# Kernel tuning notes

Hardware: AMD Instinct MI355X
Metric: run time of the kernel (lower is better)

Reference implementation:

```python
import jax, jax.numpy as jnp
import numpy as np
from jax import lax

K = 3       # kernel_conv
STRIDE = 1
PAD = 1


def setup_inputs() -> dict:
    key = jax.random.key(0)
    ks = jax.random.split(key, 11)
    b, n, H, W = 8, 64, 128, 128
    m = 64
    kk = K * K
    return {
        "x": jax.random.normal(ks[0], (b, n, H, W), jnp.float32),
        "atw1": jax.random.uniform(ks[1], (b, kk, H, W), jnp.float32),  # sigmoid-range attention1 output
        "weight": jax.random.normal(ks[2], (m, n, K, K), jnp.float32) * 0.05,
        "a2_w1": jax.random.normal(ks[3], (kk, n), jnp.float32) * 0.1,
        "a2_b1": jax.random.normal(ks[4], (kk,), jnp.float32) * 0.1,
        "a2_w2": jax.random.normal(ks[5], (kk, kk), jnp.float32) * 0.1,
        "a2_b2": jax.random.normal(ks[6], (kk,), jnp.float32) * 0.1,
        "a3_w1": jax.random.normal(ks[7], (m, n), jnp.float32) * 0.1,
        "a3_b1": jax.random.normal(ks[8], (m,), jnp.float32) * 0.1,
        "a3_w2": jax.random.normal(ks[9], (m, m), jnp.float32) * 0.1,
        "a3_b2": jax.random.normal(ks[10], (m,), jnp.float32) * 0.1,
    }


def reference(x, atw1, weight, a2_w1, a2_b1, a2_w2, a2_b2, a3_w1, a3_b1, a3_w2, a3_b2):
    b, n, H, W = x.shape
    m = weight.shape[0]
    kk = K * K
    n_H = 1 + (H + 2 * PAD - K) // STRIDE
    n_W = 1 + (W + 2 * PAD - K) // STRIDE
    P = n_H * n_W

    # F.unfold(x, k, stride, padding): [b, n*k*k, P] with channel-major ordering (c, kh, kw)
    patches = lax.conv_general_dilated_patches(
        x, (K, K), (STRIDE, STRIDE), [(PAD, PAD), (PAD, PAD)])  # [b, n*kk, n_H, n_W]
    kx = patches.reshape(b, n, kk, P)

    # attention2: global avg pool + two 1x1 convs -> per-batch per-tap ratio [b, kk]
    g = x.mean(axis=(2, 3))                                   # [b, n]
    ratio = jax.nn.relu(g @ a2_w1.T + a2_b1) @ a2_w2.T + a2_b2  # [b, kk]

    # per-pixel per-tap weight (broadcast over input channels, as the torch repeat/view does)
    a = atw1.reshape(b, kk, P) * ratio[:, :, None]            # [b, kk, P]
    wx = kx * a[:, None, :, :]                                # [b, n, kk, P]

    # dynamic-weighted im2col matmul with static conv weight
    w = weight.reshape(m, n, kk)
    y = jnp.einsum('bctp,mct->bmp', wx, w)                    # [b, m, P]

    # attention3 bias: global avg pool + two 1x1 convs -> [b, m]
    bias = jax.nn.relu(g @ a3_w1.T + a3_b1) @ a3_w2.T + a3_b2
    y = y + bias[:, :, None]

    # F.fold with kernel 1 is a reshape back to the spatial grid
    return y.reshape(b, m, n_H, n_W)
```

## Files before the change

### kernel.cpp

```cpp
#include <hip/hip_runtime.h>

typedef __attribute__((ext_vector_type(8))) short short8;
typedef __attribute__((ext_vector_type(4))) float f32x4;

#define HH 128
#define WW 128
#define TW 16
#define TH 4
#define HALOW 18
#define HALOH 6
#define NPIX (HALOW * HALOH)
#define NGROUP (TH / 2)

__device__ inline unsigned short f2bf(float f) {
    unsigned int u = __builtin_bit_cast(unsigned int, f);
    u += 0x7fffu + ((u >> 16) & 1u);
    return (unsigned short)(u >> 16);
}

__global__ __launch_bounds__(256) void prep_kernel(
    const float* __restrict__ x, const float* __restrict__ wgt,
    unsigned short* __restrict__ xT, float* __restrict__ partials,
    unsigned short* __restrict__ W3) {
    const int id = blockIdx.x;
    const int tid = threadIdx.x;
    {
        int i = id * 256 + tid;
        if (i < 64 * 64 * 9) {
            int j = i & 7, rest = i >> 3;
            int m = rest & 63; rest >>= 6;
            int lk = rest & 3; rest >>= 2;
            int ks = rest & 1, t = rest >> 1;
            int c = ks * 32 + lk * 8 + j;
            W3[i] = f2bf(wgt[(m * 64 + c) * 9 + t]);
        }
    }
    const int b = id & 7, pt = id >> 3;
    const int p0 = pt * 64;
    __shared__ unsigned int lt[64 * 33];
    __shared__ float red[8][32][2];

    const int px = tid & 63, cp0 = tid >> 6;
    const float* xb = x + (size_t)b * 64 * (HH * WW) + p0 + px;
    #pragma unroll
    for (int i = 0; i < 8; ++i) {
        int cp = cp0 + 4 * i;
        float v0 = xb[(size_t)(2 * cp) * (HH * WW)];
        float v1 = xb[(size_t)(2 * cp + 1) * (HH * WW)];
        lt[px * 33 + cp] = (unsigned)f2bf(v0) | ((unsigned)f2bf(v1) << 16);
    }
    __syncthreads();
    #pragma unroll
    for (int it = 0; it < 2; ++it) {
        int idx = it * 256 + tid;
        int p = idx >> 3, ch = idx & 7;
        int o = p * 33 + ch * 4;
        uint4 v = make_uint4(lt[o], lt[o + 1], lt[o + 2], lt[o + 3]);
        *(uint4*)(xT + ((size_t)(b * (HH * WW) + p0 + p) * 64 + ch * 8)) = v;
    }
    {
        int cp = tid & 31, grp = tid >> 5;
        float s0 = 0.f, s1 = 0.f;
        #pragma unroll
        for (int j2 = 0; j2 < 8; ++j2) {
            unsigned u = lt[(grp * 8 + j2) * 33 + cp];
            s0 += __builtin_bit_cast(float, u << 16);
            s1 += __builtin_bit_cast(float, u & 0xffff0000u);
        }
        red[grp][cp][0] = s0;
        red[grp][cp][1] = s1;
    }
    __syncthreads();
    if (tid < 64) {
        float s = 0.f;
        #pragma unroll
        for (int g2 = 0; g2 < 8; ++g2) s += red[g2][tid >> 1][tid & 1];
        partials[(size_t)(b * 256 + pt) * 64 + tid] = s;
    }
}

__global__ __launch_bounds__(256) void mlp_kernel(
    const float* __restrict__ partials,
    const float* __restrict__ a2w1, const float* __restrict__ a2b1,
    const float* __restrict__ a2w2, const float* __restrict__ a2b2,
    const float* __restrict__ a3w1, const float* __restrict__ a3b1,
    const float* __restrict__ a3w2, const float* __restrict__ a3b2,
    float* __restrict__ ratio, float* __restrict__ bias) {
    int b = blockIdx.x;
    int tid = threadIdx.x;
    int t = tid & 63, is = tid >> 6;
    float s = 0.f;
    #pragma unroll 8
    for (int k = 0; k < 64; ++k)
        s += partials[(size_t)(b * 256 + is + 4 * k) * 64 + t];
    __shared__ float rb[4][64];
    __shared__ float gs[64], h2[9], h3[64];
    rb[is][t] = s;
    __syncthreads();
    if (tid < 64)
        gs[t] = (rb[0][t] + rb[1][t] + rb[2][t] + rb[3][t]) * (1.f / (HH * WW));
    __syncthreads();
    if (tid < 64) {
        float s3 = 0.f;
        #pragma unroll 8
        for (int i = 0; i < 64; ++i) s3 += gs[i] * a3w1[t * 64 + i];
        h3[t] = fmaxf(s3 + a3b1[t], 0.f);
        if (t < 9) {
            float s2 = 0.f;
            #pragma unroll 8
            for (int i = 0; i < 64; ++i) s2 += gs[i] * a2w1[t * 64 + i];
            h2[t] = fmaxf(s2 + a2b1[t], 0.f);
        }
    }
    __syncthreads();
    if (tid < 64) {
        float o = 0.f;
        #pragma unroll 8
        for (int i = 0; i < 64; ++i) o += h3[i] * a3w2[t * 64 + i];
        bias[b * 64 + t] = o + a3b2[t];
        if (t < 9) {
            float r = 0.f;
            #pragma unroll
            for (int i = 0; i < 9; ++i) r += h2[i] * a2w2[t * 9 + i];
            ratio[b * 9 + t] = r + a2b2[t];
        }
    }
}

__global__ __launch_bounds__(256, 4) void main_kernel(
    const unsigned short* __restrict__ xT, const float* __restrict__ atw1,
    const unsigned short* __restrict__ W3, const float* __restrict__ ratio,
    const float* __restrict__ bias, float* __restrict__ out) {
    const int id = blockIdx.x;
    const int b = id & 7;
    const int rem = id >> 3;
    const int tY = rem >> 3;
    const int tX = rem & 7;
    const int tid = threadIdx.x;
    const int lane = tid & 63;
    const int wtile = tid >> 6;
    const int lm = lane & 15;
    const int lk = lane >> 4;
    const int px0 = tX * TW, py0 = tY * TH;

    __shared__ char xsc[NPIX * 128];
    __shared__ float alds[9][TH][TW];

    #pragma unroll
    for (int it = 0; it < 4; ++it) {
        int idx = it * 256 + tid;
        if (idx < NPIX * 8) {
            int pix = idx >> 3, ch = idx & 7;
            int yy = pix / HALOW;
            int xx = pix - yy * HALOW;
            int gy = py0 + yy - 1, gx = px0 + xx - 1;
            uint4 v = make_uint4(0u, 0u, 0u, 0u);
            if (gy >= 0 && gy < HH && gx >= 0 && gx < WW)
                v = *(const uint4*)(xT + ((size_t)((b * HH + gy) * WW + gx) * 64 + ch * 8));
            *(uint4*)(xsc + pix * 128 + ((ch * 16) ^ ((pix & 7) << 4))) = v;
        }
    }

    #pragma unroll
    for (int i = tid; i < 9 * TH * TW; i += 256) {
        int t = i / (TH * TW);
        int rem2 = i - t * (TH * TW);
        int rr = rem2 >> 4, cc = rem2 & 15;
        alds[0][0][i] = atw1[((size_t)(b * 9 + t) * HH + py0 + rr) * WW + px0 + cc]
                        * ratio[b * 9 + t];
    }

    short8 wfrag[9][2];
    {
        const short8* W3v = (const short8*)W3;
        #pragma unroll
        for (int t = 0; t < 9; ++t)
            #pragma unroll
            for (int ks = 0; ks < 2; ++ks)
                wfrag[t][ks] = W3v[(((t * 2 + ks) * 4 + lk) * 64) + wtile * 16 + lm];
    }

    float biasr[4];
    #pragma unroll
    for (int q = 0; q < 4; ++q) biasr[q] = bias[b * 64 + wtile * 16 + lk * 4 + q];

    __syncthreads();

    #pragma unroll 1
    for (int g2 = 0; g2 < NGROUP; ++g2) {
        const int r0 = g2 * 2;
        float av[2][9];
        #pragma unroll
        for (int rr = 0; rr < 2; ++rr)
            #pragma unroll
            for (int t = 0; t < 9; ++t) av[rr][t] = alds[t][r0 + rr][lm];

        f32x4 yac[2];
        #pragma unroll
        for (int rr = 0; rr < 2; ++rr) yac[rr] = (f32x4){0.f, 0.f, 0.f, 0.f};

        #pragma unroll
        for (int hl = 0; hl < 4; ++hl) {
            const int pixr = (r0 + hl) * HALOW + lm;
            short8 bf[3][2];
            #pragma unroll
            for (int dx = 0; dx < 3; ++dx) {
                const int pix = pixr + dx;
                const int sw = (pix & 7) << 4;
                const char* bp2 = xsc + pix * 128;
                #pragma unroll
                for (int ks = 0; ks < 2; ++ks)
                    bf[dx][ks] = __builtin_bit_cast(short8,
                        *(const uint4*)(bp2 + ((ks * 64 + lk * 16) ^ sw)));
            }
            #pragma unroll
            for (int dy = 0; dy < 3; ++dy) {
                const int r = hl - dy;
                if (r < 0 || r > 1) continue;
                #pragma unroll
                for (int dx = 0; dx < 3; ++dx) {
                    const int t = dy * 3 + dx;
                    f32x4 z = {0.f, 0.f, 0.f, 0.f};
                    z = __builtin_amdgcn_mfma_f32_16x16x32_bf16(wfrag[t][0], bf[dx][0], z, 0, 0, 0);
                    z = __builtin_amdgcn_mfma_f32_16x16x32_bf16(wfrag[t][1], bf[dx][1], z, 0, 0, 0);
                    #pragma unroll
                    for (int q = 0; q < 4; ++q) yac[r][q] = fmaf(av[r][t], z[q], yac[r][q]);
                }
            }
        }
        #pragma unroll
        for (int rr = 0; rr < 2; ++rr) {
            const int pyg = py0 + r0 + rr;
            #pragma unroll
            for (int q = 0; q < 4; ++q) {
                int m = wtile * 16 + lk * 4 + q;
                out[((size_t)(b * 64 + m) * HH + pyg) * WW + px0 + lm] = yac[rr][q] + biasr[q];
            }
        }
    }
}

extern "C" void kernel_launch(void* const* d_in, const int* in_sizes, int n_in,
                              void* d_out, int out_size, void* d_ws, size_t ws_size,
                              hipStream_t stream) {
    const float* x    = (const float*)d_in[0];
    const float* atw1 = (const float*)d_in[1];
    const float* wgt  = (const float*)d_in[2];
    const float* a2w1 = (const float*)d_in[3];
    const float* a2b1 = (const float*)d_in[4];
    const float* a2w2 = (const float*)d_in[5];
    const float* a2b2 = (const float*)d_in[6];
    const float* a3w1 = (const float*)d_in[7];
    const float* a3b1 = (const float*)d_in[8];
    const float* a3w2 = (const float*)d_in[9];
    const float* a3b2 = (const float*)d_in[10];
    float* out = (float*)d_out;

    float* ws = (float*)d_ws;
    float* ratio = ws;
    float* bias  = ws + 128;
    unsigned short* W3 = (unsigned short*)(ws + 1024);
    float* partials = ws + 19456;
    unsigned short* xT = (unsigned short*)(ws + 150528);

    prep_kernel<<<dim3(2048), dim3(256), 0, stream>>>(x, wgt, xT, partials, W3);
    mlp_kernel<<<dim3(8), dim3(256), 0, stream>>>(partials, a2w1, a2b1, a2w2, a2b2,
                                                  a3w1, a3b1, a3w2, a3b2, ratio, bias);
    main_kernel<<<dim3(2048), dim3(256), 0, stream>>>(xT, atw1, W3, ratio, bias, out);
}
```

Baseline: 44.04 us.

## Replace LDS halo tiling with direct global loads over persistent row-strip tasks

Removes the shared-memory halo tile and the atw1 staging buffer. Each block now loops over four 1x16-pixel row tasks and loads the 3x3 neighbourhood of bf16 channels straight from global memory, relying on L1/L2 to supply the halo reuse. The weight fragments are loaded once per block and reused across four tasks, and the occupancy hint drops from 4 to 3 blocks per SM. The trade is more global or cache traffic and longer load latency for each MFMA, since the halo data is re-read three times per row instead of once from LDS.

```diff
diff --git a/kernel.cpp b/kernel.cpp
--- a/kernel.cpp
+++ b/kernel.cpp
@@ -5,12 +5,6 @@
 
 #define HH 128
 #define WW 128
-#define TW 16
-#define TH 4
-#define HALOW 18
-#define HALOH 6
-#define NPIX (HALOW * HALOH)
-#define NGROUP (TH / 2)
 
 __device__ inline unsigned short f2bf(float f) {
     unsigned int u = __builtin_bit_cast(unsigned int, f);
@@ -127,48 +121,18 @@
     }
 }
 
-__global__ __launch_bounds__(256, 4) void main_kernel(
+__global__ __launch_bounds__(256, 3) void main_kernel(
     const unsigned short* __restrict__ xT, const float* __restrict__ atw1,
     const unsigned short* __restrict__ W3, const float* __restrict__ ratio,
     const float* __restrict__ bias, float* __restrict__ out) {
     const int id = blockIdx.x;
     const int b = id & 7;
-    const int rem = id >> 3;
-    const int tY = rem >> 3;
-    const int tX = rem & 7;
+    const int j = id >> 3;
     const int tid = threadIdx.x;
     const int lane = tid & 63;
     const int wtile = tid >> 6;
     const int lm = lane & 15;
     const int lk = lane >> 4;
-    const int px0 = tX * TW, py0 = tY * TH;
-
-    __shared__ char xsc[NPIX * 128];
-    __shared__ float alds[9][TH][TW];
-
-    #pragma unroll
-    for (int it = 0; it < 4; ++it) {
-        int idx = it * 256 + tid;
-        if (idx < NPIX * 8) {
-            int pix = idx >> 3, ch = idx & 7;
-            int yy = pix / HALOW;
-            int xx = pix - yy * HALOW;
-            int gy = py0 + yy - 1, gx = px0 + xx - 1;
-            uint4 v = make_uint4(0u, 0u, 0u, 0u);
-            if (gy >= 0 && gy < HH && gx >= 0 && gx < WW)
-                v = *(const uint4*)(xT + ((size_t)((b * HH + gy) * WW + gx) * 64 + ch * 8));
-            *(uint4*)(xsc + pix * 128 + ((ch * 16) ^ ((pix & 7) << 4))) = v;
-        }
-    }
-
-    #pragma unroll
-    for (int i = tid; i < 9 * TH * TW; i += 256) {
-        int t = i / (TH * TW);
-        int rem2 = i - t * (TH * TW);
-        int rr = rem2 >> 4, cc = rem2 & 15;
-        alds[0][0][i] = atw1[((size_t)(b * 9 + t) * HH + py0 + rr) * WW + px0 + cc]
-                        * ratio[b * 9 + t];
-    }
 
     short8 wfrag[9][2];
     {
@@ -179,64 +143,64 @@
             for (int ks = 0; ks < 2; ++ks)
                 wfrag[t][ks] = W3v[(((t * 2 + ks) * 4 + lk) * 64) + wtile * 16 + lm];
     }
-
+    float rat[9];
+    #pragma unroll
+    for (int t = 0; t < 9; ++t) rat[t] = ratio[b * 9 + t];
     float biasr[4];
     #pragma unroll
     for (int q = 0; q < 4; ++q) biasr[q] = bias[b * 64 + wtile * 16 + lk * 4 + q];
 
-    __syncthreads();
+    const unsigned short* xb = xT + (size_t)b * (HH * WW) * 64;
+    const float* ab = atw1 + (size_t)b * 9 * (HH * WW);
+    float* ob = out + (size_t)b * 64 * (HH * WW);
 
     #pragma unroll 1
-    for (int g2 = 0; g2 < NGROUP; ++g2) {
-        const int r0 = g2 * 2;
-        float av[2][9];
-        #pragma unroll
-        for (int rr = 0; rr < 2; ++rr)
-            #pragma unroll
-            for (int t = 0; t < 9; ++t) av[rr][t] = alds[t][r0 + rr][lm];
-
-        f32x4 yac[2];
-        #pragma unroll
-        for (int rr = 0; rr < 2; ++rr) yac[rr] = (f32x4){0.f, 0.f, 0.f, 0.f};
-
-        #pragma unroll
-        for (int hl = 0; hl < 4; ++hl) {
-            const int pixr = (r0 + hl) * HALOW + lm;
+    for (int it = 0; it < 4; ++it) {
+        const int task = j + it * 256;
+        const int y = task >> 3;
+        const int x0 = (task & 7) * 16;
+        const int gx = x0 + lm;
+
+        float av[9];
+        #pragma unroll
+        for (int t = 0; t < 9; ++t)
+            av[t] = ab[(size_t)t * (HH * WW) + y * WW + gx] * rat[t];
+
+        f32x4 yac = {0.f, 0.f, 0.f, 0.f};
+
+        #pragma unroll
+        for (int dy = 0; dy < 3; ++dy) {
+            const int gy = y + dy - 1;
+            const bool rowok = (gy >= 0) && (gy < HH);
             short8 bf[3][2];
             #pragma unroll
             for (int dx = 0; dx < 3; ++dx) {
-                const int pix = pixr + dx;
-                const int sw = (pix & 7) << 4;
-                const char* bp2 = xsc + pix * 128;
+                const int gxx = gx + dx - 1;
+                const bool ok = rowok && (gxx >= 0) && (gxx < WW);
+                const uint4* p = (const uint4*)(xb + (size_t)(gy * WW + gxx) * 64);
                 #pragma unroll
-                for (int ks = 0; ks < 2; ++ks)
-                    bf[dx][ks] = __builtin_bit_cast(short8,
-                        *(const uint4*)(bp2 + ((ks * 64 + lk * 16) ^ sw)));
-            }
-            #pragma unroll
-            for (int dy = 0; dy < 3; ++dy) {
-                const int r = hl - dy;
-                if (r < 0 || r > 1) continue;
-                #pragma unroll
-                for (int dx = 0; dx < 3; ++dx) {
-                    const int t = dy * 3 + dx;
-                    f32x4 z = {0.f, 0.f, 0.f, 0.f};
-                    z = __builtin_amdgcn_mfma_f32_16x16x32_bf16(wfrag[t][0], bf[dx][0], z, 0, 0, 0);
-                    z = __builtin_amdgcn_mfma_f32_16x16x32_bf16(wfrag[t][1], bf[dx][1], z, 0, 0, 0);
-                    #pragma unroll
-                    for (int q = 0; q < 4; ++q) yac[r][q] = fmaf(av[r][t], z[q], yac[r][q]);
+                for (int ks = 0; ks < 2; ++ks) {
+                    uint4 v = make_uint4(0u, 0u, 0u, 0u);
+                    if (ok) v = p[ks * 4 + lk];
+                    bf[dx][ks] = __builtin_bit_cast(short8, v);
                 }
             }
-        }
-        #pragma unroll
-        for (int rr = 0; rr < 2; ++rr) {
-            const int pyg = py0 + r0 + rr;
-            #pragma unroll
-            for (int q = 0; q < 4; ++q) {
-                int m = wtile * 16 + lk * 4 + q;
-                out[((size_t)(b * 64 + m) * HH + pyg) * WW + px0 + lm] = yac[rr][q] + biasr[q];
+            #pragma unroll
+            for (int dx = 0; dx < 3; ++dx) {
+                const int t = dy * 3 + dx;
+                f32x4 z = {0.f, 0.f, 0.f, 0.f};
+                z = __builtin_amdgcn_mfma_f32_16x16x32_bf16(wfrag[t][0], bf[dx][0], z, 0, 0, 0);
+                z = __builtin_amdgcn_mfma_f32_16x16x32_bf16(wfrag[t][1], bf[dx][1], z, 0, 0, 0);
+                #pragma unroll
+                for (int q = 0; q < 4; ++q) yac[q] = fmaf(av[t], z[q], yac[q]);
             }
         }
+        #pragma unroll
+        for (int q = 0; q < 4; ++q) {
+            int m = wtile * 16 + lk * 4 + q;
+            ob[((size_t)m * HH + y) * WW + gx] = yac[q] + biasr[q];
+        }
+        __builtin_amdgcn_s_barrier();
     }
 }
 
```

Result: slower. 99.33 us (+125.6%).

## Make main kernel persistent over four tiles with register-staged double buffering

Applied to the files above, without the earlier changes.

Each block of the main kernel now processes four consecutive spatial tiles instead of one, and the grid shrinks to 512 blocks. The next tile's input halo and attention weights are prefetched into registers while MFMAs run on the current tile, then written to a second LDS buffer. This is meant to hide global load latency and amortise the per-block weight-fragment and bias loads. In exchange, LDS use doubles, the launch bound drops to 2 blocks per CU, and the small grid may underfill the CUs.

```diff
diff --git a/kernel.cpp b/kernel.cpp
--- a/kernel.cpp
+++ b/kernel.cpp
@@ -10,7 +10,8 @@
 #define HALOW 18
 #define HALOH 6
 #define NPIX (HALOW * HALOH)
-#define NGROUP (TH / 2)
+#define XSB (NPIX * 128)
+#define NA (9 * TH * TW)
 
 __device__ inline unsigned short f2bf(float f) {
     unsigned int u = __builtin_bit_cast(unsigned int, f);
@@ -127,48 +128,21 @@
     }
 }
 
-__global__ __launch_bounds__(256, 4) void main_kernel(
+__global__ __launch_bounds__(256, 2) void main_kernel(
     const unsigned short* __restrict__ xT, const float* __restrict__ atw1,
     const unsigned short* __restrict__ W3, const float* __restrict__ ratio,
     const float* __restrict__ bias, float* __restrict__ out) {
     const int id = blockIdx.x;
     const int b = id & 7;
-    const int rem = id >> 3;
-    const int tY = rem >> 3;
-    const int tX = rem & 7;
+    const int j = id >> 3;
     const int tid = threadIdx.x;
     const int lane = tid & 63;
     const int wtile = tid >> 6;
     const int lm = lane & 15;
     const int lk = lane >> 4;
-    const int px0 = tX * TW, py0 = tY * TH;
-
-    __shared__ char xsc[NPIX * 128];
-    __shared__ float alds[9][TH][TW];
-
-    #pragma unroll
-    for (int it = 0; it < 4; ++it) {
-        int idx = it * 256 + tid;
-        if (idx < NPIX * 8) {
-            int pix = idx >> 3, ch = idx & 7;
-            int yy = pix / HALOW;
-            int xx = pix - yy * HALOW;
-            int gy = py0 + yy - 1, gx = px0 + xx - 1;
-            uint4 v = make_uint4(0u, 0u, 0u, 0u);
-            if (gy >= 0 && gy < HH && gx >= 0 && gx < WW)
-                v = *(const uint4*)(xT + ((size_t)((b * HH + gy) * WW + gx) * 64 + ch * 8));
-            *(uint4*)(xsc + pix * 128 + ((ch * 16) ^ ((pix & 7) << 4))) = v;
-        }
-    }
-
-    #pragma unroll
-    for (int i = tid; i < 9 * TH * TW; i += 256) {
-        int t = i / (TH * TW);
-        int rem2 = i - t * (TH * TW);
-        int rr = rem2 >> 4, cc = rem2 & 15;
-        alds[0][0][i] = atw1[((size_t)(b * 9 + t) * HH + py0 + rr) * WW + px0 + cc]
-                        * ratio[b * 9 + t];
-    }
+
+    __shared__ char xsc[2][XSB];
+    __shared__ float alds[2][NA];
 
     short8 wfrag[9][2];
     {
@@ -179,64 +153,130 @@
             for (int ks = 0; ks < 2; ++ks)
                 wfrag[t][ks] = W3v[(((t * 2 + ks) * 4 + lk) * 64) + wtile * 16 + lm];
     }
-
     float biasr[4];
     #pragma unroll
     for (int q = 0; q < 4; ++q) biasr[q] = bias[b * 64 + wtile * 16 + lk * 4 + q];
 
+    const unsigned short* xb = xT + (size_t)b * (HH * WW) * 64;
+    const float* ab = atw1 + (size_t)b * 9 * (HH * WW);
+    const float* rg = ratio + b * 9;
+    float* ob = out + (size_t)b * 64 * (HH * WW);
+
+    uint4 sx[4];
+    float sa[3];
+
+    auto LOADT = [&](int task) {
+        const int py0 = (task >> 3) * TH, px0 = (task & 7) * TW;
+        #pragma unroll
+        for (int i = 0; i < 4; ++i) {
+            int idx = i * 256 + tid;
+            uint4 v = make_uint4(0u, 0u, 0u, 0u);
+            if (idx < NPIX * 8) {
+                int pix = idx >> 3, ch = idx & 7;
+                int yy = pix / HALOW;
+                int xx = pix - yy * HALOW;
+                int gy = py0 + yy - 1, gx = px0 + xx - 1;
+                if (gy >= 0 && gy < HH && gx >= 0 && gx < WW)
+                    v = *(const uint4*)(xb + ((size_t)(gy * WW + gx) * 64 + ch * 8));
+            }
+            sx[i] = v;
+        }
+        #pragma unroll
+        for (int i = 0; i < 3; ++i) {
+            int idx = i * 256 + tid;
+            float v = 0.f;
+            if (idx < NA) {
+                int t = idx >> 6, rem = idx & 63;
+                int rr = rem >> 4, cc = rem & 15;
+                v = ab[(size_t)t * (HH * WW) + (py0 + rr) * WW + px0 + cc] * rg[t];
+            }
+            sa[i] = v;
+        }
+    };
+    auto DSWRITE = [&](int bi) {
+        #pragma unroll
+        for (int i = 0; i < 4; ++i) {
+            int idx = i * 256 + tid;
+            if (idx < NPIX * 8) {
+                int pix = idx >> 3, ch = idx & 7;
+                *(uint4*)(&xsc[bi][pix * 128 + ((ch * 16) ^ ((pix & 7) << 4))]) = sx[i];
+            }
+        }
+        #pragma unroll
+        for (int i = 0; i < 3; ++i) {
+            int idx = i * 256 + tid;
+            if (idx < NA) alds[bi][idx] = sa[i];
+        }
+    };
+
+    LOADT(j * 4);
+    DSWRITE(0);
     __syncthreads();
 
     #pragma unroll 1
-    for (int g2 = 0; g2 < NGROUP; ++g2) {
-        const int r0 = g2 * 2;
-        float av[2][9];
-        #pragma unroll
-        for (int rr = 0; rr < 2; ++rr)
-            #pragma unroll
-            for (int t = 0; t < 9; ++t) av[rr][t] = alds[t][r0 + rr][lm];
-
-        f32x4 yac[2];
-        #pragma unroll
-        for (int rr = 0; rr < 2; ++rr) yac[rr] = (f32x4){0.f, 0.f, 0.f, 0.f};
-
-        #pragma unroll
-        for (int hl = 0; hl < 4; ++hl) {
-            const int pixr = (r0 + hl) * HALOW + lm;
-            short8 bf[3][2];
-            #pragma unroll
-            for (int dx = 0; dx < 3; ++dx) {
-                const int pix = pixr + dx;
-                const int sw = (pix & 7) << 4;
-                const char* bp2 = xsc + pix * 128;
+    for (int it = 0; it < 4; ++it) {
+        if (it < 3) LOADT(j * 4 + it + 1);
+
+        const int task = j * 4 + it;
+        const int py0 = (task >> 3) * TH, px0 = (task & 7) * TW;
+        const char* xs = xsc[it & 1];
+        const float* al = alds[it & 1];
+
+        #pragma unroll
+        for (int g2 = 0; g2 < 2; ++g2) {
+            const int r0 = g2 * 2;
+            float av[2][9];
+            #pragma unroll
+            for (int rr = 0; rr < 2; ++rr)
                 #pragma unroll
-                for (int ks = 0; ks < 2; ++ks)
-                    bf[dx][ks] = __builtin_bit_cast(short8,
-                        *(const uint4*)(bp2 + ((ks * 64 + lk * 16) ^ sw)));
-            }
-            #pragma unroll
-            for (int dy = 0; dy < 3; ++dy) {
-                const int r = hl - dy;
-                if (r < 0 || r > 1) continue;
+                for (int t = 0; t < 9; ++t) av[rr][t] = al[t * 64 + (r0 + rr) * 16 + lm];
+
+            f32x4 yac[2];
+            #pragma unroll
+            for (int rr = 0; rr < 2; ++rr) yac[rr] = (f32x4){0.f, 0.f, 0.f, 0.f};
+
+            #pragma unroll
+            for (int hl = 0; hl < 4; ++hl) {
+                const int pixr = (r0 + hl) * HALOW + lm;
+                short8 bf[3][2];
                 #pragma unroll
                 for (int dx = 0; dx < 3; ++dx) {
-                    const int t = dy * 3 + dx;
-                    f32x4 z = {0.f, 0.f, 0.f, 0.f};
-                    z = __builtin_amdgcn_mfma_f32_16x16x32_bf16(wfrag[t][0], bf[dx][0], z, 0, 0, 0);
-                    z = __builtin_amdgcn_mfma_f32_16x16x32_bf16(wfrag[t][1], bf[dx][1], z, 0, 0, 0);
+                    const int pix = pixr + dx;
+                    const int sw = (pix & 7) << 4;
+                    const char* bp2 = xs + pix * 128;
                     #pragma unroll
-                    for (int q = 0; q < 4; ++q) yac[r][q] = fmaf(av[r][t], z[q], yac[r][q]);
+                    for (int ks = 0; ks < 2; ++ks)
+                        bf[dx][ks] = __builtin_bit_cast(short8,
+                            *(const uint4*)(bp2 + ((ks * 64 + lk * 16) ^ sw)));
                 }
-            }
-        }
-        #pragma unroll
-        for (int rr = 0; rr < 2; ++rr) {
-            const int pyg = py0 + r0 + rr;
-            #pragma unroll
-            for (int q = 0; q < 4; ++q) {
-                int m = wtile * 16 + lk * 4 + q;
-                out[((size_t)(b * 64 + m) * HH + pyg) * WW + px0 + lm] = yac[rr][q] + biasr[q];
-            }
-        }
+                #pragma unroll
+                for (int dy = 0; dy < 3; ++dy) {
+                    const int r = hl - dy;
+                    if (r < 0 || r > 1) continue;
+                    #pragma unroll
+                    for (int dx = 0; dx < 3; ++dx) {
+                        const int t = dy * 3 + dx;
+                        f32x4 z = {0.f, 0.f, 0.f, 0.f};
+                        z = __builtin_amdgcn_mfma_f32_16x16x32_bf16(wfrag[t][0], bf[dx][0], z, 0, 0, 0);
+                        z = __builtin_amdgcn_mfma_f32_16x16x32_bf16(wfrag[t][1], bf[dx][1], z, 0, 0, 0);
+                        #pragma unroll
+                        for (int q = 0; q < 4; ++q) yac[r][q] = fmaf(av[r][t], z[q], yac[r][q]);
+                    }
+                }
+            }
+            #pragma unroll
+            for (int rr = 0; rr < 2; ++rr) {
+                const int pyg = py0 + r0 + rr;
+                #pragma unroll
+                for (int q = 0; q < 4; ++q) {
+                    int m = wtile * 16 + lk * 4 + q;
+                    ob[((size_t)m * HH + pyg) * WW + px0 + lm] = yac[rr][q] + biasr[q];
+                }
+            }
+        }
+
+        if (it < 3) DSWRITE((it + 1) & 1);
+        __syncthreads();
     }
 }
 
@@ -266,5 +306,5 @@
     prep_kernel<<<dim3(2048), dim3(256), 0, stream>>>(x, wgt, xT, partials, W3);
     mlp_kernel<<<dim3(8), dim3(256), 0, stream>>>(partials, a2w1, a2b1, a2w2, a2b2,
                                                   a3w1, a3b1, a3w2, a3b2, ratio, bias);
-    main_kernel<<<dim3(2048), dim3(256), 0, stream>>>(xT, atw1, W3, ratio, bias, out);
-}
+    main_kernel<<<dim3(512), dim3(256), 0, stream>>>(xT, atw1, W3, ratio, bias, out);
+}
```

Result: faster. 41.83 us (-5.0%).

## Switch main conv kernel to 32x32x16 MFMA with wider 32x4 pixel tiles

Applied to the files above, without the earlier changes.

Rewrites the main kernel to use 32x32x16 bf16 MFMA instead of 16x16x32. Each block now covers a 32-wide by 4-tall pixel tile, with waves split into two output-channel halves and two row pairs, and the grid shrinks to 1024 blocks. The conv weights are repacked into a layout matching the new fragment shape. The aim is to cut halo overhead, issue fewer larger MFMAs and reuse each LDS load more. In exchange, register pressure rises (36 weight fragments per lane, launch bounds lowered to 2 blocks) and fewer blocks are available for latency hiding.

```diff
diff --git a/kernel.cpp b/kernel.cpp
--- a/kernel.cpp
+++ b/kernel.cpp
@@ -1,16 +1,13 @@
 #include <hip/hip_runtime.h>
 
 typedef __attribute__((ext_vector_type(8))) short short8;
-typedef __attribute__((ext_vector_type(4))) float f32x4;
+typedef __attribute__((ext_vector_type(16))) float f32x16;
 
 #define HH 128
 #define WW 128
-#define TW 16
-#define TH 4
-#define HALOW 18
+#define HALOW 34
 #define HALOH 6
 #define NPIX (HALOW * HALOH)
-#define NGROUP (TH / 2)
 
 __device__ inline unsigned short f2bf(float f) {
     unsigned int u = __builtin_bit_cast(unsigned int, f);
@@ -21,18 +18,19 @@
 __global__ __launch_bounds__(256) void prep_kernel(
     const float* __restrict__ x, const float* __restrict__ wgt,
     unsigned short* __restrict__ xT, float* __restrict__ partials,
-    unsigned short* __restrict__ W3) {
+    unsigned short* __restrict__ W4) {
     const int id = blockIdx.x;
     const int tid = threadIdx.x;
     {
         int i = id * 256 + tid;
         if (i < 64 * 64 * 9) {
-            int j = i & 7, rest = i >> 3;
-            int m = rest & 63; rest >>= 6;
-            int lk = rest & 3; rest >>= 2;
-            int ks = rest & 1, t = rest >> 1;
-            int c = ks * 32 + lk * 8 + j;
-            W3[i] = f2bf(wgt[(m * 64 + c) * 9 + t]);
+            int j = i & 7;
+            int m = (i >> 3) & 63;
+            int hi = (i >> 9) & 1;
+            int s = (i >> 10) & 3;
+            int t = i >> 12;
+            int c = s * 16 + hi * 8 + j;
+            W4[i] = f2bf(wgt[(m * 64 + c) * 9 + t]);
         }
     }
     const int b = id & 7, pt = id >> 3;
@@ -127,115 +125,117 @@
     }
 }
 
-__global__ __launch_bounds__(256, 4) void main_kernel(
+__global__ __launch_bounds__(256, 2) void main_kernel(
     const unsigned short* __restrict__ xT, const float* __restrict__ atw1,
-    const unsigned short* __restrict__ W3, const float* __restrict__ ratio,
+    const unsigned short* __restrict__ W4, const float* __restrict__ ratio,
     const float* __restrict__ bias, float* __restrict__ out) {
     const int id = blockIdx.x;
     const int b = id & 7;
-    const int rem = id >> 3;
-    const int tY = rem >> 3;
-    const int tX = rem & 7;
+    const int j = id >> 3;
+    const int tX = j & 3, tY = j >> 2;
+    const int px0 = tX * 32, py0 = tY * 4;
     const int tid = threadIdx.x;
     const int lane = tid & 63;
-    const int wtile = tid >> 6;
-    const int lm = lane & 15;
-    const int lk = lane >> 4;
-    const int px0 = tX * TW, py0 = tY * TH;
+    const int w = tid >> 6;
+    const int wm = w >> 1;
+    const int wr = w & 1;
+    const int lp = lane & 31;
+    const int hi = lane >> 5;
 
     __shared__ char xsc[NPIX * 128];
-    __shared__ float alds[9][TH][TW];
-
-    #pragma unroll
-    for (int it = 0; it < 4; ++it) {
-        int idx = it * 256 + tid;
-        if (idx < NPIX * 8) {
-            int pix = idx >> 3, ch = idx & 7;
-            int yy = pix / HALOW;
-            int xx = pix - yy * HALOW;
-            int gy = py0 + yy - 1, gx = px0 + xx - 1;
-            uint4 v = make_uint4(0u, 0u, 0u, 0u);
-            if (gy >= 0 && gy < HH && gx >= 0 && gx < WW)
-                v = *(const uint4*)(xT + ((size_t)((b * HH + gy) * WW + gx) * 64 + ch * 8));
-            *(uint4*)(xsc + pix * 128 + ((ch * 16) ^ ((pix & 7) << 4))) = v;
-        }
-    }
-
-    #pragma unroll
-    for (int i = tid; i < 9 * TH * TW; i += 256) {
-        int t = i / (TH * TW);
-        int rem2 = i - t * (TH * TW);
-        int rr = rem2 >> 4, cc = rem2 & 15;
-        alds[0][0][i] = atw1[((size_t)(b * 9 + t) * HH + py0 + rr) * WW + px0 + cc]
-                        * ratio[b * 9 + t];
-    }
-
-    short8 wfrag[9][2];
-    {
-        const short8* W3v = (const short8*)W3;
+    __shared__ float alds[9][4][32];
+
+    {
+        const unsigned short* xb = xT + (size_t)b * (HH * WW) * 64;
+        #pragma unroll
+        for (int it2 = 0; it2 < 7; ++it2) {
+            int idx = it2 * 256 + tid;
+            if (idx < NPIX * 8) {
+                int pix = idx >> 3, ch = idx & 7;
+                int yy = pix / HALOW;
+                int xx = pix - yy * HALOW;
+                int gy = py0 + yy - 1, gx = px0 + xx - 1;
+                uint4 v = make_uint4(0u, 0u, 0u, 0u);
+                if (gy >= 0 && gy < HH && gx >= 0 && gx < WW)
+                    v = *(const uint4*)(xb + ((size_t)(gy * WW + gx) * 64 + ch * 8));
+                *(uint4*)(xsc + pix * 128 + ((ch * 16) ^ ((pix & 7) << 4))) = v;
+            }
+        }
+    }
+    {
+        const float* ab = atw1 + (size_t)b * 9 * (HH * WW);
+        #pragma unroll
+        for (int i0 = 0; i0 < 5; ++i0) {
+            int i = i0 * 256 + tid;
+            if (i < 9 * 4 * 32) {
+                int t = i >> 7, rem = i & 127;
+                int rr = rem >> 5, cc = rem & 31;
+                alds[t][rr][cc] =
+                    ab[(size_t)t * (HH * WW) + (py0 + rr) * WW + px0 + cc] * ratio[b * 9 + t];
+            }
+        }
+    }
+    short8 wfrag[9][4];
+    {
+        const short8* W4v = (const short8*)W4;
         #pragma unroll
         for (int t = 0; t < 9; ++t)
             #pragma unroll
-            for (int ks = 0; ks < 2; ++ks)
-                wfrag[t][ks] = W3v[(((t * 2 + ks) * 4 + lk) * 64) + wtile * 16 + lm];
-    }
-
-    float biasr[4];
-    #pragma unroll
-    for (int q = 0; q < 4; ++q) biasr[q] = bias[b * 64 + wtile * 16 + lk * 4 + q];
-
-    __syncthreads();
-
-    #pragma unroll 1
-    for (int g2 = 0; g2 < NGROUP; ++g2) {
-        const int r0 = g2 * 2;
-        float av[2][9];
-        #pragma unroll
-        for (int rr = 0; rr < 2; ++rr)
-            #pragma unroll
-            for (int t = 0; t < 9; ++t) av[rr][t] = alds[t][r0 + rr][lm];
-
-        f32x4 yac[2];
-        #pragma unroll
-        for (int rr = 0; rr < 2; ++rr) yac[rr] = (f32x4){0.f, 0.f, 0.f, 0.f};
-
-        #pragma unroll
-        for (int hl = 0; hl < 4; ++hl) {
-            const int pixr = (r0 + hl) * HALOW + lm;
-            short8 bf[3][2];
-            #pragma unroll
-            for (int dx = 0; dx < 3; ++dx) {
-                const int pix = pixr + dx;
-                const int sw = (pix & 7) << 4;
-                const char* bp2 = xsc + pix * 128;
+            for (int s = 0; s < 4; ++s)
+                wfrag[t][s] = W4v[((t * 4 + s) * 2 + hi) * 64 + wm * 32 + lp];
+    }
+    __syncthreads();
+
+    f32x16 yac0, yac1;
+    #pragma unroll
+    for (int q = 0; q < 16; ++q) { yac0[q] = 0.f; yac1[q] = 0.f; }
+
+    #pragma unroll
+    for (int hl = 0; hl < 4; ++hl) {
+        const int hrow = wr * 2 + hl;
+        #pragma unroll
+        for (int dx = 0; dx < 3; ++dx) {
+            const int pix = hrow * HALOW + lp + dx;
+            const int sw = (pix & 7) << 4;
+            const char* bp = xsc + pix * 128;
+            short8 bf[4];
+            #pragma unroll
+            for (int s = 0; s < 4; ++s)
+                bf[s] = __builtin_bit_cast(short8,
+                        *(const uint4*)(bp + ((s * 32 + hi * 16) ^ sw)));
+            #pragma unroll
+            for (int rr = 0; rr < 2; ++rr) {
+                const int dy = hl - rr;
+                if (dy < 0 || dy > 2) continue;
+                const int t = dy * 3 + dx;
+                f32x16 z;
                 #pragma unroll
-                for (int ks = 0; ks < 2; ++ks)
-                    bf[dx][ks] = __builtin_bit_cast(short8,
-                        *(const uint4*)(bp2 + ((ks * 64 + lk * 16) ^ sw)));
-            }
-            #pragma unroll
-            for (int dy = 0; dy < 3; ++dy) {
-                const int r = hl - dy;
-                if (r < 0 || r > 1) continue;
+                for (int q = 0; q < 16; ++q) z[q] = 0.f;
                 #pragma unroll
-                for (int dx = 0; dx < 3; ++dx) {
-                    const int t = dy * 3 + dx;
-                    f32x4 z = {0.f, 0.f, 0.f, 0.f};
-                    z = __builtin_amdgcn_mfma_f32_16x16x32_bf16(wfrag[t][0], bf[dx][0], z, 0, 0, 0);
-                    z = __builtin_amdgcn_mfma_f32_16x16x32_bf16(wfrag[t][1], bf[dx][1], z, 0, 0, 0);
+                for (int s = 0; s < 4; ++s)
+                    z = __builtin_amdgcn_mfma_f32_32x32x16_bf16(wfrag[t][s], bf[s], z, 0, 0, 0);
+                const float a = alds[t][wr * 2 + rr][lp];
+                if (rr == 0) {
                     #pragma unroll
-                    for (int q = 0; q < 4; ++q) yac[r][q] = fmaf(av[r][t], z[q], yac[r][q]);
+                    for (int q = 0; q < 16; ++q) yac0[q] = fmaf(a, z[q], yac0[q]);
+                } else {
+                    #pragma unroll
+                    for (int q = 0; q < 16; ++q) yac1[q] = fmaf(a, z[q], yac1[q]);
                 }
             }
         }
-        #pragma unroll
-        for (int rr = 0; rr < 2; ++rr) {
-            const int pyg = py0 + r0 + rr;
-            #pragma unroll
-            for (int q = 0; q < 4; ++q) {
-                int m = wtile * 16 + lk * 4 + q;
-                out[((size_t)(b * 64 + m) * HH + pyg) * WW + px0 + lm] = yac[rr][q] + biasr[q];
-            }
+    }
+
+    float* ob = out + (size_t)b * 64 * (HH * WW);
+    const float* bb = bias + b * 64;
+    #pragma unroll
+    for (int rr = 0; rr < 2; ++rr) {
+        const int y = py0 + wr * 2 + rr;
+        #pragma unroll
+        for (int q = 0; q < 16; ++q) {
+            const int m = wm * 32 + 4 * hi + (q & 3) + 8 * (q >> 2);
+            const float v = (rr ? yac1[q] : yac0[q]) + bb[m];
+            ob[((size_t)m * HH + y) * WW + px0 + lp] = v;
         }
     }
 }
@@ -259,12 +259,12 @@
     float* ws = (float*)d_ws;
     float* ratio = ws;
     float* bias  = ws + 128;
-    unsigned short* W3 = (unsigned short*)(ws + 1024);
+    unsigned short* W4 = (unsigned short*)(ws + 1024);
     float* partials = ws + 19456;
     unsigned short* xT = (unsigned short*)(ws + 150528);
 
-    prep_kernel<<<dim3(2048), dim3(256), 0, stream>>>(x, wgt, xT, partials, W3);
+    prep_kernel<<<dim3(2048), dim3(256), 0, stream>>>(x, wgt, xT, partials, W4);
     mlp_kernel<<<dim3(8), dim3(256), 0, stream>>>(partials, a2w1, a2b1, a2w2, a2b2,
                                                   a3w1, a3b1, a3w2, a3b2, ratio, bias);
-    main_kernel<<<dim3(2048), dim3(256), 0, stream>>>(xT, atw1, W3, ratio, bias, out);
-}
+    main_kernel<<<dim3(1024), dim3(256), 0, stream>>>(xT, atw1, W4, ratio, bias, out);
+}
```

New measurement: 49.88 us. 13.3% more time.
